# Optimization experiments

Hardware: AMD Instinct MI355X
Metric: run time of the kernel (lower is better)

## Reference

```python
import jax, jax.numpy as jnp
import numpy as np

B, S, D, H = 4, 2048, 1024, 16
HD = D // H
TEMP = 0.5
EPS = 1e-5


def setup_inputs() -> dict:
    key = jax.random.key(0)
    ks = jax.random.split(key, 9)
    s = 1.0 / np.sqrt(D)
    # weights stored as [in, out] (equivalent to torch Linear W.T)
    return {
        "x": jax.random.normal(ks[0], (B, S, D), dtype=jnp.float32),
        "Wq": jax.random.uniform(ks[1], (D, D), minval=-s, maxval=s),
        "bq": jnp.zeros((D,), jnp.float32),
        "Wk": jax.random.uniform(ks[2], (D, D), minval=-s, maxval=s),
        "bk": jnp.zeros((D,), jnp.float32),
        "Wv": jax.random.uniform(ks[3], (D, D), minval=-s, maxval=s),
        "bv": jnp.zeros((D,), jnp.float32),
        "Wo": jax.random.uniform(ks[4], (D, D), minval=-s, maxval=s),
        "bo": jnp.zeros((D,), jnp.float32),
        "ln_g": jnp.ones((D,), jnp.float32),
        "ln_b": jnp.zeros((D,), jnp.float32),
    }


def reference(x, Wq, bq, Wk, bk, Wv, bv, Wo, bo, ln_g, ln_b):
    # projections -> [B, H, S, HD]
    def proj(W, b):
        return (x @ W + b).reshape(B, S, H, HD).transpose(0, 2, 1, 3)

    Q, K, V = proj(Wq, bq), proj(Wk, bk), proj(Wv, bv)
    scale = 1.0 / (np.sqrt(HD) * TEMP)
    scores = jnp.einsum("bhqd,bhkd->bhqk", Q, K) * scale  # [B,H,S,S]
    attn = jax.nn.softmax(scores, axis=-1)  # dropout p=0 -> identity
    ctx = jnp.einsum("bhqk,bhkd->bhqd", attn, V)
    ctx = ctx.transpose(0, 2, 1, 3).reshape(B, S, D)
    out = ctx @ Wo + bo
    # layernorm(out + residual)
    h = out + x
    mu = h.mean(axis=-1, keepdims=True)
    var = h.var(axis=-1, keepdims=True)
    out = (h - mu) / jnp.sqrt(var + EPS) * ln_g + ln_b
    avg_attention = attn.mean(axis=1)  # [B, S, S]
    return out, avg_attention
```

## Files before the change

### kernel.cpp

```cpp
#include <hip/hip_runtime.h>

#define DEV static __device__ __forceinline__

typedef float f32x4 __attribute__((ext_vector_type(4)));
typedef __bf16 bf16x8 __attribute__((ext_vector_type(8)));
typedef unsigned short u16x8 __attribute__((ext_vector_type(8)));
typedef unsigned short u16x4 __attribute__((ext_vector_type(4)));
typedef unsigned u32x2 __attribute__((ext_vector_type(2)));

static constexpr float SCALE_LOG2E = 0.25f * 1.4426950408889634f;

DEV unsigned short f2bf(float f) {
  return __builtin_bit_cast(unsigned short, (__bf16)f);
}

DEV unsigned pk2(float a, float b) {
  unsigned short lo = f2bf(a), hi = f2bf(b);
  return (unsigned)lo | ((unsigned)hi << 16);
}

DEV f32x4 fzero() { f32x4 z; z[0] = z[1] = z[2] = z[3] = 0.f; return z; }

DEV void gll16(const void* g, void* l) {
  __builtin_amdgcn_global_load_lds((__attribute__((address_space(1))) void*)g,
                                   (__attribute__((address_space(3))) void*)l, 16, 0, 0);
}

DEV f32x4 mfma16(bf16x8 a, bf16x8 b, f32x4 c) {
  return __builtin_amdgcn_mfma_f32_16x16x32_bf16(a, b, c, 0, 0, 0);
}

__global__ __launch_bounds__(256) void k_cvt_x(const float* __restrict__ x,
                                               unsigned short* __restrict__ xb, int n) {
  int i = (blockIdx.x * 256 + threadIdx.x) * 4;
  if (i < n) {
    f32x4 v = *(const f32x4*)(x + i);
    u16x4 o;
    o[0] = f2bf(v[0]); o[1] = f2bf(v[1]); o[2] = f2bf(v[2]); o[3] = f2bf(v[3]);
    *(u16x4*)(xb + i) = o;
  }
}

__global__ __launch_bounds__(256) void k_cvt_wT(const float* __restrict__ w0,
                                                const float* __restrict__ w1,
                                                const float* __restrict__ w2,
                                                const float* __restrict__ w3,
                                                unsigned short* __restrict__ wt) {
  __shared__ float t[32][33];
  const float* w = blockIdx.z == 0 ? w0 : blockIdx.z == 1 ? w1 : blockIdx.z == 2 ? w2 : w3;
  unsigned short* dst = wt + (size_t)blockIdx.z * 1024 * 1024;
  int n0 = blockIdx.x * 32, k0 = blockIdx.y * 32;
  int tx = threadIdx.x, ty = threadIdx.y;
#pragma unroll
  for (int i = 0; i < 4; ++i)
    t[ty + 8 * i][tx] = w[(size_t)(k0 + ty + 8 * i) * 1024 + n0 + tx];
  __syncthreads();
#pragma unroll
  for (int i = 0; i < 4; ++i)
    dst[(size_t)(n0 + ty + 8 * i) * 1024 + k0 + tx] = f2bf(t[tx][ty + 8 * i]);
}

template <int MODE>
__global__ __launch_bounds__(256) void k_gemm(
    const unsigned short* __restrict__ A, const unsigned short* __restrict__ Bt,
    unsigned short* __restrict__ oq, unsigned short* __restrict__ ok,
    unsigned short* __restrict__ ov, const float* __restrict__ biasq,
    const float* __restrict__ biask, const float* __restrict__ biasv,
    float* __restrict__ outh, const float* __restrict__ xres,
    const float* __restrict__ biaso) {
  __shared__ unsigned short As[128 * 64];
  __shared__ unsigned short Bs[128 * 64];
  const int tid = threadIdx.x;
  const int w = tid >> 6, ln = tid & 63;
  const int kg = ln >> 4, l15 = ln & 15;
  const int wm = w >> 1, wn = w & 1;
  const long arow0 = (long)blockIdx.y * 128;
  const long brow0 = (long)blockIdx.x * 128;

  f32x4 acc[4][4];
#pragma unroll
  for (int m = 0; m < 4; ++m) {
#pragma unroll
    for (int n = 0; n < 4; ++n) acc[m][n] = fzero();
  }

  for (int kt = 0; kt < 16; ++kt) {
    __syncthreads();
#pragma unroll
    for (int rnd = 0; rnd < 4; ++rnd) {
      int slot = rnd * 256 + tid;
      int r = slot >> 3, ch = slot & 7;
      int gch = ch ^ (r & 7);
      gll16(A + (arow0 + r) * 1024 + kt * 64 + gch * 8, (char*)As + slot * 16);
      gll16(Bt + (brow0 + r) * 1024 + kt * 64 + gch * 8, (char*)Bs + slot * 16);
    }
    __syncthreads();
#pragma unroll
    for (int kk = 0; kk < 2; ++kk) {
      bf16x8 af[4], bfr[4];
#pragma unroll
      for (int m = 0; m < 4; ++m) {
        int row = wm * 64 + m * 16 + l15;
        int bir = (kk * 64 + kg * 16) ^ ((row & 7) << 4);
        af[m] = *(const bf16x8*)((const char*)As + row * 128 + bir);
      }
#pragma unroll
      for (int n = 0; n < 4; ++n) {
        int row = wn * 64 + n * 16 + l15;
        int bir = (kk * 64 + kg * 16) ^ ((row & 7) << 4);
        bfr[n] = *(const bf16x8*)((const char*)Bs + row * 128 + bir);
      }
#pragma unroll
      for (int m = 0; m < 4; ++m) {
#pragma unroll
        for (int n = 0; n < 4; ++n) acc[m][n] = mfma16(af[m], bfr[n], acc[m][n]);
      }
    }
  }

#pragma unroll
  for (int n = 0; n < 4; ++n) {
    int col = (int)brow0 + wn * 64 + n * 16 + l15;
    if (MODE == 0) {
      int which = col >> 10, nn = col & 1023;
      int hh = nn >> 6, dd = nn & 63;
      unsigned short* dst = which == 0 ? oq : which == 1 ? ok : ov;
      const float* bp = which == 0 ? biasq : which == 1 ? biask : biasv;
      float bias = bp[nn];
#pragma unroll
      for (int m = 0; m < 4; ++m) {
        int row0 = (int)arow0 + wm * 64 + m * 16 + kg * 4;
#pragma unroll
        for (int r = 0; r < 4; ++r) {
          int row = row0 + r;
          int bb = row >> 11, ss = row & 2047;
          dst[(((long)(bb * 16 + hh)) * 2048 + ss) * 64 + dd] =
              f2bf(acc[m][n][r] + bias);
        }
      }
    } else {
      float bias = biaso[col];
#pragma unroll
      for (int m = 0; m < 4; ++m) {
        long row0 = arow0 + wm * 64 + m * 16 + kg * 4;
#pragma unroll
        for (int r = 0; r < 4; ++r) {
          long row = row0 + r;
          outh[row * 1024 + col] = acc[m][n][r] + bias + xres[row * 1024 + col];
        }
      }
    }
  }
}

__global__ __launch_bounds__(256, 4) void k_flash(
    const unsigned short* __restrict__ Q, const unsigned short* __restrict__ K,
    const unsigned short* __restrict__ V, unsigned short* __restrict__ ctx,
    float* __restrict__ mrow, float* __restrict__ lrow) {
  __shared__ unsigned short Ks[64 * 64];
  __shared__ unsigned short Vt[64 * 64];
  __shared__ unsigned short Ps[4][16 * 64];
  const int tid = threadIdx.x, w = tid >> 6, ln = tid & 63;
  const int kg = ln >> 4, l15 = ln & 15;
  const int qt = blockIdx.x, hh = blockIdx.y, bb = blockIdx.z;
  const long bh = (long)bb * 16 + hh;
  const unsigned short* Qg = Q + bh * 2048 * 64;
  const unsigned short* Kg = K + bh * 2048 * 64;
  const unsigned short* Vg = V + bh * 2048 * 64;

  const int qrow = qt * 64 + w * 16 + l15;
  bf16x8 qf[2];
  qf[0] = *(const bf16x8*)(Qg + (long)qrow * 64 + kg * 8);
  qf[1] = *(const bf16x8*)(Qg + (long)qrow * 64 + 32 + kg * 8);

  f32x4 oacc[4];
#pragma unroll
  for (int nf = 0; nf < 4; ++nf) oacc[nf] = fzero();
  float m_run = -1e30f, l_run = 0.f;

  char* pw = (char*)Ps[w] + l15 * 128;
  const int swz = (l15 & 7) << 4;

  for (int kt = 0; kt < 32; ++kt) {
    __syncthreads();
#pragma unroll
    for (int rnd = 0; rnd < 2; ++rnd) {
      int slot = rnd * 256 + tid;
      int r = slot >> 3, ch = slot & 7;
      int gch = ch ^ (r & 7);
      gll16(Kg + ((long)kt * 64 + r) * 64 + gch * 8, (char*)Ks + slot * 16);
    }
    {
      int kp = tid & 31, ch = tid >> 5;
      int r0 = kp * 2;
      u16x8 v0 = *(const u16x8*)(Vg + ((long)kt * 64 + r0) * 64 + ch * 8);
      u16x8 v1 = *(const u16x8*)(Vg + ((long)kt * 64 + r0 + 1) * 64 + ch * 8);
#pragma unroll
      for (int i = 0; i < 8; ++i) {
        int c = ch * 8 + i;
        unsigned val = (unsigned)v0[i] | ((unsigned)v1[i] << 16);
        *(unsigned*)((char*)Vt + c * 128 + ((r0 * 2) ^ ((c & 7) << 4))) = val;
      }
    }
    __syncthreads();

    f32x4 st[4];
#pragma unroll
    for (int nf = 0; nf < 4; ++nf) st[nf] = fzero();
#pragma unroll
    for (int kk = 0; kk < 2; ++kk) {
#pragma unroll
      for (int nf = 0; nf < 4; ++nf) {
        int row = nf * 16 + l15;
        int bir = (kk * 64 + kg * 16) ^ ((row & 7) << 4);
        bf16x8 kb = *(const bf16x8*)((const char*)Ks + row * 128 + bir);
        st[nf] = mfma16(kb, qf[kk], st[nf]);
      }
    }

    float mx0 = fmaxf(fmaxf(st[0][0], st[0][1]), fmaxf(st[0][2], st[0][3]));
    float mx1 = fmaxf(fmaxf(st[1][0], st[1][1]), fmaxf(st[1][2], st[1][3]));
    float mx2 = fmaxf(fmaxf(st[2][0], st[2][1]), fmaxf(st[2][2], st[2][3]));
    float mx3 = fmaxf(fmaxf(st[3][0], st[3][1]), fmaxf(st[3][2], st[3][3]));
    float mx = fmaxf(fmaxf(mx0, mx1), fmaxf(mx2, mx3));
    mx = fmaxf(mx, __shfl_xor(mx, 16));
    mx = fmaxf(mx, __shfl_xor(mx, 32));
    mx *= SCALE_LOG2E;
    float mnew = fmaxf(m_run, mx);
    float alpha = exp2f(m_run - mnew);
    m_run = mnew;

    float sum = 0.f;
#pragma unroll
    for (int nf = 0; nf < 4; ++nf) {
      float p0 = exp2f(st[nf][0] * SCALE_LOG2E - m_run);
      float p1 = exp2f(st[nf][1] * SCALE_LOG2E - m_run);
      float p2 = exp2f(st[nf][2] * SCALE_LOG2E - m_run);
      float p3 = exp2f(st[nf][3] * SCALE_LOG2E - m_run);
      st[nf][0] = p0; st[nf][1] = p1; st[nf][2] = p2; st[nf][3] = p3;
      sum += (p0 + p1) + (p2 + p3);
    }
    sum += __shfl_xor(sum, 16);
    sum += __shfl_xor(sum, 32);
    l_run = l_run * alpha + sum;

#pragma unroll
    for (int nf = 0; nf < 4; ++nf) {
      u32x2 pv2;
      pv2[0] = pk2(st[nf][0], st[nf][1]);
      pv2[1] = pk2(st[nf][2], st[nf][3]);
      *(u32x2*)(pw + ((nf * 32 + kg * 8) ^ swz)) = pv2;
    }

#pragma unroll
    for (int nf = 0; nf < 4; ++nf) oacc[nf] *= alpha;

#pragma unroll
    for (int kk = 0; kk < 2; ++kk) {
      bf16x8 pb = *(const bf16x8*)(pw + ((kk * 64 + kg * 16) ^ swz));
#pragma unroll
      for (int nf = 0; nf < 4; ++nf) {
        int dd = nf * 16 + l15;
        int bir2 = (kk * 64 + kg * 16) ^ ((dd & 7) << 4);
        bf16x8 vb = *(const bf16x8*)((const char*)Vt + dd * 128 + bir2);
        oacc[nf] = mfma16(vb, pb, oacc[nf]);
      }
    }
  }

  float linv = 1.0f / l_run;
#pragma unroll
  for (int nf = 0; nf < 4; ++nf) {
    u16x4 o;
#pragma unroll
    for (int r = 0; r < 4; ++r) o[r] = f2bf(oacc[nf][r] * linv);
    *(u16x4*)(ctx + ((long)bb * 2048 + qrow) * 1024 + hh * 64 + nf * 16 + kg * 4) = o;
  }
  if (kg == 0) {
    mrow[bh * 2048 + qrow] = m_run;
    lrow[bh * 2048 + qrow] = l_run;
  }
}

__global__ __launch_bounds__(256) void k_avg(
    const unsigned short* __restrict__ Q, const unsigned short* __restrict__ K,
    const float* __restrict__ mrow, const float* __restrict__ lrow,
    float* __restrict__ avg) {
  __shared__ unsigned short Qs[64 * 64];
  __shared__ unsigned short Ks[64 * 64];
  const int tid = threadIdx.x, w = tid >> 6, ln = tid & 63;
  const int kg = ln >> 4, l15 = ln & 15;
  const int kt = blockIdx.x, qt = blockIdx.y, bb = blockIdx.z;

  f32x4 aacc[4];
#pragma unroll
  for (int nf = 0; nf < 4; ++nf) aacc[nf] = fzero();

  for (int hh = 0; hh < 16; ++hh) {
    const long bh = (long)bb * 16 + hh;
    const unsigned short* Qg = Q + bh * 2048 * 64;
    const unsigned short* Kg = K + bh * 2048 * 64;
    __syncthreads();
#pragma unroll
    for (int rnd = 0; rnd < 2; ++rnd) {
      int slot = rnd * 256 + tid;
      int r = slot >> 3, ch = slot & 7;
      int gch = ch ^ (r & 7);
      gll16(Qg + ((long)qt * 64 + r) * 64 + gch * 8, (char*)Qs + slot * 16);
      gll16(Kg + ((long)kt * 64 + r) * 64 + gch * 8, (char*)Ks + slot * 16);
    }
    __syncthreads();

    f32x4 sc[4];
#pragma unroll
    for (int nf = 0; nf < 4; ++nf) sc[nf] = fzero();
#pragma unroll
    for (int kk = 0; kk < 2; ++kk) {
      int arow = w * 16 + l15;
      int bir = (kk * 64 + kg * 16) ^ ((arow & 7) << 4);
      bf16x8 aq = *(const bf16x8*)((const char*)Qs + arow * 128 + bir);
#pragma unroll
      for (int nf = 0; nf < 4; ++nf) {
        int krow = nf * 16 + l15;
        int bir2 = (kk * 64 + kg * 16) ^ ((krow & 7) << 4);
        bf16x8 kb = *(const bf16x8*)((const char*)Ks + krow * 128 + bir2);
        sc[nf] = mfma16(aq, kb, sc[nf]);
      }
    }
#pragma unroll
    for (int r = 0; r < 4; ++r) {
      int qrow = qt * 64 + w * 16 + kg * 4 + r;
      float m = mrow[bh * 2048 + qrow];
      float linv = 1.0f / lrow[bh * 2048 + qrow];
#pragma unroll
      for (int nf = 0; nf < 4; ++nf)
        aacc[nf][r] += exp2f(sc[nf][r] * SCALE_LOG2E - m) * linv;
    }
  }
#pragma unroll
  for (int nf = 0; nf < 4; ++nf) {
#pragma unroll
    for (int r = 0; r < 4; ++r) {
      int qrow = qt * 64 + w * 16 + kg * 4 + r;
      int kcol = kt * 64 + nf * 16 + l15;
      avg[((long)bb * 2048 + qrow) * 2048 + kcol] = aacc[nf][r] * 0.0625f;
    }
  }
}

__global__ __launch_bounds__(256) void k_ln(float* __restrict__ io,
                                            const float* __restrict__ g,
                                            const float* __restrict__ bvec) {
  __shared__ float red[8];
  long row = blockIdx.x;
  float* p = io + row * 1024;
  int tid = threadIdx.x;
  f32x4 v = *(const f32x4*)(p + tid * 4);
  float s = v[0] + v[1] + v[2] + v[3];
  float ss = v[0] * v[0] + v[1] * v[1] + v[2] * v[2] + v[3] * v[3];
#pragma unroll
  for (int m = 1; m < 64; m <<= 1) {
    s += __shfl_xor(s, m);
    ss += __shfl_xor(ss, m);
  }
  int w = tid >> 6;
  if ((tid & 63) == 0) { red[w * 2] = s; red[w * 2 + 1] = ss; }
  __syncthreads();
  s = red[0] + red[2] + red[4] + red[6];
  ss = red[1] + red[3] + red[5] + red[7];
  float mu = s * (1.0f / 1024.0f);
  float var = ss * (1.0f / 1024.0f) - mu * mu;
  float rs = rsqrtf(var + 1e-5f);
  f32x4 o;
#pragma unroll
  for (int i = 0; i < 4; ++i) {
    int c = tid * 4 + i;
    o[i] = (v[i] - mu) * rs * g[c] + bvec[c];
  }
  *(f32x4*)(p + tid * 4) = o;
}

extern "C" void kernel_launch(void* const* d_in, const int* in_sizes, int n_in,
                              void* d_out, int out_size, void* d_ws, size_t ws_size,
                              hipStream_t stream) {
  (void)in_sizes; (void)n_in; (void)out_size; (void)ws_size;
  const float* x  = (const float*)d_in[0];
  const float* Wq = (const float*)d_in[1];
  const float* bq = (const float*)d_in[2];
  const float* Wk = (const float*)d_in[3];
  const float* bk = (const float*)d_in[4];
  const float* Wv = (const float*)d_in[5];
  const float* bv = (const float*)d_in[6];
  const float* Wo = (const float*)d_in[7];
  const float* bo = (const float*)d_in[8];
  const float* lg = (const float*)d_in[9];
  const float* lb = (const float*)d_in[10];
  float* out = (float*)d_out;
  float* avg = out + (long)8192 * 1024;

  char* ws = (char*)d_ws;
  unsigned short* xb  = (unsigned short*)(ws);
  unsigned short* wt  = (unsigned short*)(ws + ((size_t)16 << 20));
  unsigned short* Qb  = (unsigned short*)(ws + ((size_t)24 << 20));
  unsigned short* Kb  = (unsigned short*)(ws + ((size_t)40 << 20));
  unsigned short* Vb  = (unsigned short*)(ws + ((size_t)56 << 20));
  unsigned short* ctx = (unsigned short*)(ws + ((size_t)72 << 20));
  float* mrow = (float*)(ws + ((size_t)88 << 20));
  float* lrow = (float*)(ws + ((size_t)88 << 20) + ((size_t)1 << 19));

  k_cvt_x<<<dim3(8192), dim3(256), 0, stream>>>(x, xb, 8192 * 1024);
  k_cvt_wT<<<dim3(32, 32, 4), dim3(32, 8), 0, stream>>>(Wq, Wk, Wv, Wo, wt);
  k_gemm<0><<<dim3(24, 64), dim3(256), 0, stream>>>(
      xb, wt, Qb, Kb, Vb, bq, bk, bv, nullptr, nullptr, nullptr);
  k_flash<<<dim3(32, 16, 4), dim3(256), 0, stream>>>(Qb, Kb, Vb, ctx, mrow, lrow);
  k_avg<<<dim3(32, 32, 4), dim3(256), 0, stream>>>(Qb, Kb, mrow, lrow, avg);
  k_gemm<1><<<dim3(8, 64), dim3(256), 0, stream>>>(
      ctx, wt + (size_t)3 * 1024 * 1024, nullptr, nullptr, nullptr, nullptr, nullptr,
      nullptr, out, x, bo);
  k_ln<<<dim3(8192), dim3(256), 0, stream>>>(out, lg, lb);
}
```

Baseline: 516.4 us.

## Pre-transpose V, remap blocks across XCDs, and streamline flash/avg kernels

A separate kernel transposes V into a global [d, s] layout, so the flash kernel can fill LDS with async global_load_lds instead of a register transpose each tile. All grids become 1D, with block indices remapped so neighbouring tiles land on the same XCD for L2 reuse. The avg kernel loads Q fragments straight to registers instead of through LDS, precomputes 1/16 into the reciprocal, writes vectorised f32x4 stores and declares higher occupancy. exp2f is replaced by the hardware exp2 builtin, at the cost of an extra kernel launch and extra V traffic.

```diff
diff --git a/kernel.cpp b/kernel.cpp
--- a/kernel.cpp
+++ b/kernel.cpp
@@ -13,19 +13,17 @@
 DEV unsigned short f2bf(float f) {
   return __builtin_bit_cast(unsigned short, (__bf16)f);
 }
-
 DEV unsigned pk2(float a, float b) {
   unsigned short lo = f2bf(a), hi = f2bf(b);
   return (unsigned)lo | ((unsigned)hi << 16);
 }
-
+DEV float ex2(float x) { return __builtin_amdgcn_exp2f(x); }
 DEV f32x4 fzero() { f32x4 z; z[0] = z[1] = z[2] = z[3] = 0.f; return z; }
 
 DEV void gll16(const void* g, void* l) {
   __builtin_amdgcn_global_load_lds((__attribute__((address_space(1))) void*)g,
                                    (__attribute__((address_space(3))) void*)l, 16, 0, 0);
 }
-
 DEV f32x4 mfma16(bf16x8 a, bf16x8 b, f32x4 c) {
   return __builtin_amdgcn_mfma_f32_16x16x32_bf16(a, b, c, 0, 0, 0);
 }
@@ -60,6 +58,21 @@
     dst[(size_t)(n0 + ty + 8 * i) * 1024 + k0 + tx] = f2bf(t[tx][ty + 8 * i]);
 }
 
+__global__ __launch_bounds__(256) void k_vT(const unsigned short* __restrict__ V,
+                                            unsigned short* __restrict__ Vt) {
+  const long base = (long)blockIdx.y * 131072;
+  const int s0 = blockIdx.x * 64;
+  const int s = threadIdx.x & 63, dg = threadIdx.x >> 6;
+  const unsigned short* src = V + base + (long)(s0 + s) * 64 + dg * 16;
+  u16x8 a = *(const u16x8*)(src);
+  u16x8 b = *(const u16x8*)(src + 8);
+  unsigned short* dst = Vt + base + (long)(dg * 16) * 2048 + s0 + s;
+#pragma unroll
+  for (int i = 0; i < 8; ++i) dst[(long)i * 2048] = a[i];
+#pragma unroll
+  for (int i = 0; i < 8; ++i) dst[(long)(8 + i) * 2048] = b[i];
+}
+
 template <int MODE>
 __global__ __launch_bounds__(256) void k_gemm(
     const unsigned short* __restrict__ A, const unsigned short* __restrict__ Bt,
@@ -67,22 +80,23 @@
     unsigned short* __restrict__ ov, const float* __restrict__ biasq,
     const float* __restrict__ biask, const float* __restrict__ biasv,
     float* __restrict__ outh, const float* __restrict__ xres,
-    const float* __restrict__ biaso) {
+    const float* __restrict__ biaso, int nx) {
   __shared__ unsigned short As[128 * 64];
   __shared__ unsigned short Bs[128 * 64];
   const int tid = threadIdx.x;
   const int w = tid >> 6, ln = tid & 63;
   const int kg = ln >> 4, l15 = ln & 15;
   const int wm = w >> 1, wn = w & 1;
-  const long arow0 = (long)blockIdx.y * 128;
-  const long brow0 = (long)blockIdx.x * 128;
+  const int chunk = gridDim.x >> 3;
+  const int lin = (blockIdx.x & 7) * chunk + (blockIdx.x >> 3);
+  const long arow0 = (long)(lin / nx) * 128;
+  const long brow0 = (long)(lin % nx) * 128;
 
   f32x4 acc[4][4];
 #pragma unroll
-  for (int m = 0; m < 4; ++m) {
+  for (int m = 0; m < 4; ++m)
 #pragma unroll
     for (int n = 0; n < 4; ++n) acc[m][n] = fzero();
-  }
 
   for (int kt = 0; kt < 16; ++kt) {
     __syncthreads();
@@ -111,10 +125,9 @@
         bfr[n] = *(const bf16x8*)((const char*)Bs + row * 128 + bir);
       }
 #pragma unroll
-      for (int m = 0; m < 4; ++m) {
+      for (int m = 0; m < 4; ++m)
 #pragma unroll
         for (int n = 0; n < 4; ++n) acc[m][n] = mfma16(af[m], bfr[n], acc[m][n]);
-      }
     }
   }
 
@@ -155,68 +168,68 @@
 
 __global__ __launch_bounds__(256, 4) void k_flash(
     const unsigned short* __restrict__ Q, const unsigned short* __restrict__ K,
-    const unsigned short* __restrict__ V, unsigned short* __restrict__ ctx,
+    const unsigned short* __restrict__ Vtg, unsigned short* __restrict__ ctx,
     float* __restrict__ mrow, float* __restrict__ lrow) {
   __shared__ unsigned short Ks[64 * 64];
   __shared__ unsigned short Vt[64 * 64];
   __shared__ unsigned short Ps[4][16 * 64];
   const int tid = threadIdx.x, w = tid >> 6, ln = tid & 63;
   const int kg = ln >> 4, l15 = ln & 15;
-  const int qt = blockIdx.x, hh = blockIdx.y, bb = blockIdx.z;
+  const int lin = (blockIdx.x & 7) * 256 + (blockIdx.x >> 3);
+  const int qt = lin & 31, hh = (lin >> 5) & 15, bb = lin >> 9;
   const long bh = (long)bb * 16 + hh;
-  const unsigned short* Qg = Q + bh * 2048 * 64;
-  const unsigned short* Kg = K + bh * 2048 * 64;
-  const unsigned short* Vg = V + bh * 2048 * 64;
-
+  const unsigned short* Qg = Q + bh * 131072;
   const int qrow = qt * 64 + w * 16 + l15;
-  bf16x8 qf[2];
-  qf[0] = *(const bf16x8*)(Qg + (long)qrow * 64 + kg * 8);
-  qf[1] = *(const bf16x8*)(Qg + (long)qrow * 64 + 32 + kg * 8);
+  const bf16x8 qf0 = *(const bf16x8*)(Qg + (long)qrow * 64 + kg * 8);
+  const bf16x8 qf1 = *(const bf16x8*)(Qg + (long)qrow * 64 + 32 + kg * 8);
+
+  const int r0 = tid >> 3, gch = (tid & 7) ^ (r0 & 7);
+  const unsigned short* kp0 = K + bh * 131072 + r0 * 64 + gch * 8;
+  const unsigned short* kp1 = kp0 + 32 * 64;
+  const unsigned short* vp0 = Vtg + bh * 131072 + r0 * 2048 + gch * 8;
+  const unsigned short* vp1 = vp0 + 32 * 2048;
+  char* kl0 = (char*)Ks + tid * 16;
+  char* kl1 = kl0 + 4096;
+  char* vl0 = (char*)Vt + tid * 16;
+  char* vl1 = vl0 + 4096;
+
+  const int swz = (l15 & 7) << 4;
+  int bir[2];
+  bir[0] = (kg * 16) ^ swz;
+  bir[1] = (64 + kg * 16) ^ swz;
+  const char* ksb[4];
+  const char* vtb[4];
+#pragma unroll
+  for (int nf = 0; nf < 4; ++nf) {
+    ksb[nf] = (const char*)Ks + (nf * 16 + l15) * 128;
+    vtb[nf] = (const char*)Vt + (nf * 16 + l15) * 128;
+  }
+  char* pw = (char*)Ps[w] + l15 * 128;
 
   f32x4 oacc[4];
 #pragma unroll
   for (int nf = 0; nf < 4; ++nf) oacc[nf] = fzero();
   float m_run = -1e30f, l_run = 0.f;
 
-  char* pw = (char*)Ps[w] + l15 * 128;
-  const int swz = (l15 & 7) << 4;
-
   for (int kt = 0; kt < 32; ++kt) {
     __syncthreads();
-#pragma unroll
-    for (int rnd = 0; rnd < 2; ++rnd) {
-      int slot = rnd * 256 + tid;
-      int r = slot >> 3, ch = slot & 7;
-      int gch = ch ^ (r & 7);
-      gll16(Kg + ((long)kt * 64 + r) * 64 + gch * 8, (char*)Ks + slot * 16);
-    }
-    {
-      int kp = tid & 31, ch = tid >> 5;
-      int r0 = kp * 2;
-      u16x8 v0 = *(const u16x8*)(Vg + ((long)kt * 64 + r0) * 64 + ch * 8);
-      u16x8 v1 = *(const u16x8*)(Vg + ((long)kt * 64 + r0 + 1) * 64 + ch * 8);
-#pragma unroll
-      for (int i = 0; i < 8; ++i) {
-        int c = ch * 8 + i;
-        unsigned val = (unsigned)v0[i] | ((unsigned)v1[i] << 16);
-        *(unsigned*)((char*)Vt + c * 128 + ((r0 * 2) ^ ((c & 7) << 4))) = val;
-      }
-    }
+    gll16(kp0, kl0);
+    gll16(kp1, kl1);
+    gll16(vp0, vl0);
+    gll16(vp1, vl1);
+    kp0 += 4096; kp1 += 4096; vp0 += 64; vp1 += 64;
     __syncthreads();
 
     f32x4 st[4];
 #pragma unroll
     for (int nf = 0; nf < 4; ++nf) st[nf] = fzero();
 #pragma unroll
-    for (int kk = 0; kk < 2; ++kk) {
+    for (int kk = 0; kk < 2; ++kk)
 #pragma unroll
       for (int nf = 0; nf < 4; ++nf) {
-        int row = nf * 16 + l15;
-        int bir = (kk * 64 + kg * 16) ^ ((row & 7) << 4);
-        bf16x8 kb = *(const bf16x8*)((const char*)Ks + row * 128 + bir);
-        st[nf] = mfma16(kb, qf[kk], st[nf]);
-      }
-    }
+        bf16x8 kb = *(const bf16x8*)(ksb[nf] + bir[kk]);
+        st[nf] = mfma16(kb, kk ? qf1 : qf0, st[nf]);
+      }
 
     float mx0 = fmaxf(fmaxf(st[0][0], st[0][1]), fmaxf(st[0][2], st[0][3]));
     float mx1 = fmaxf(fmaxf(st[1][0], st[1][1]), fmaxf(st[1][2], st[1][3]));
@@ -227,16 +240,16 @@
     mx = fmaxf(mx, __shfl_xor(mx, 32));
     mx *= SCALE_LOG2E;
     float mnew = fmaxf(m_run, mx);
-    float alpha = exp2f(m_run - mnew);
+    float alpha = ex2(m_run - mnew);
     m_run = mnew;
 
     float sum = 0.f;
 #pragma unroll
     for (int nf = 0; nf < 4; ++nf) {
-      float p0 = exp2f(st[nf][0] * SCALE_LOG2E - m_run);
-      float p1 = exp2f(st[nf][1] * SCALE_LOG2E - m_run);
-      float p2 = exp2f(st[nf][2] * SCALE_LOG2E - m_run);
-      float p3 = exp2f(st[nf][3] * SCALE_LOG2E - m_run);
+      float p0 = ex2(st[nf][0] * SCALE_LOG2E - m_run);
+      float p1 = ex2(st[nf][1] * SCALE_LOG2E - m_run);
+      float p2 = ex2(st[nf][2] * SCALE_LOG2E - m_run);
+      float p3 = ex2(st[nf][3] * SCALE_LOG2E - m_run);
       st[nf][0] = p0; st[nf][1] = p1; st[nf][2] = p2; st[nf][3] = p3;
       sum += (p0 + p1) + (p2 + p3);
     }
@@ -257,12 +270,10 @@
 
 #pragma unroll
     for (int kk = 0; kk < 2; ++kk) {
-      bf16x8 pb = *(const bf16x8*)(pw + ((kk * 64 + kg * 16) ^ swz));
+      bf16x8 pb = *(const bf16x8*)(pw + bir[kk]);
 #pragma unroll
       for (int nf = 0; nf < 4; ++nf) {
-        int dd = nf * 16 + l15;
-        int bir2 = (kk * 64 + kg * 16) ^ ((dd & 7) << 4);
-        bf16x8 vb = *(const bf16x8*)((const char*)Vt + dd * 128 + bir2);
+        bf16x8 vb = *(const bf16x8*)(vtb[nf] + bir[kk]);
         oacc[nf] = mfma16(vb, pb, oacc[nf]);
       }
     }
@@ -282,70 +293,69 @@
   }
 }
 
-__global__ __launch_bounds__(256) void k_avg(
+__global__ __launch_bounds__(256, 4) void k_avg(
     const unsigned short* __restrict__ Q, const unsigned short* __restrict__ K,
     const float* __restrict__ mrow, const float* __restrict__ lrow,
     float* __restrict__ avg) {
-  __shared__ unsigned short Qs[64 * 64];
   __shared__ unsigned short Ks[64 * 64];
   const int tid = threadIdx.x, w = tid >> 6, ln = tid & 63;
   const int kg = ln >> 4, l15 = ln & 15;
-  const int kt = blockIdx.x, qt = blockIdx.y, bb = blockIdx.z;
+  const int lin = (blockIdx.x & 7) * 512 + (blockIdx.x >> 3);
+  const int kt = lin & 31, qt = (lin >> 5) & 31, bb = lin >> 10;
+  const int qrow = qt * 64 + w * 16 + l15;
+
+  const int r0 = tid >> 3, gch = (tid & 7) ^ (r0 & 7);
+  const unsigned short* kp0 = K + (long)bb * 16 * 131072 + kt * 4096 + r0 * 64 + gch * 8;
+  const unsigned short* kp1 = kp0 + 2048;
+  char* kl0 = (char*)Ks + tid * 16;
+  char* kl1 = kl0 + 4096;
+  const unsigned short* qp = Q + (long)bb * 16 * 131072 + (long)qrow * 64 + kg * 8;
+  const float* mp = mrow + (long)bb * 16 * 2048 + qrow;
+  const float* lp = lrow + (long)bb * 16 * 2048 + qrow;
+
+  const int swz = (l15 & 7) << 4;
+  int bir[2];
+  bir[0] = (kg * 16) ^ swz;
+  bir[1] = (64 + kg * 16) ^ swz;
+  const char* ksb[4];
+#pragma unroll
+  for (int nf = 0; nf < 4; ++nf) ksb[nf] = (const char*)Ks + (nf * 16 + l15) * 128;
 
   f32x4 aacc[4];
 #pragma unroll
   for (int nf = 0; nf < 4; ++nf) aacc[nf] = fzero();
 
   for (int hh = 0; hh < 16; ++hh) {
-    const long bh = (long)bb * 16 + hh;
-    const unsigned short* Qg = Q + bh * 2048 * 64;
-    const unsigned short* Kg = K + bh * 2048 * 64;
-    __syncthreads();
-#pragma unroll
-    for (int rnd = 0; rnd < 2; ++rnd) {
-      int slot = rnd * 256 + tid;
-      int r = slot >> 3, ch = slot & 7;
-      int gch = ch ^ (r & 7);
-      gll16(Qg + ((long)qt * 64 + r) * 64 + gch * 8, (char*)Qs + slot * 16);
-      gll16(Kg + ((long)kt * 64 + r) * 64 + gch * 8, (char*)Ks + slot * 16);
-    }
-    __syncthreads();
-
-    f32x4 sc[4];
-#pragma unroll
-    for (int nf = 0; nf < 4; ++nf) sc[nf] = fzero();
-#pragma unroll
-    for (int kk = 0; kk < 2; ++kk) {
-      int arow = w * 16 + l15;
-      int bir = (kk * 64 + kg * 16) ^ ((arow & 7) << 4);
-      bf16x8 aq = *(const bf16x8*)((const char*)Qs + arow * 128 + bir);
+    __syncthreads();
+    gll16(kp0, kl0);
+    gll16(kp1, kl1);
+    bf16x8 q0 = *(const bf16x8*)(qp);
+    bf16x8 q1 = *(const bf16x8*)(qp + 32);
+    float m = *mp;
+    float li = 0.0625f / *lp;
+    kp0 += 131072; kp1 += 131072; qp += 131072; mp += 2048; lp += 2048;
+    __syncthreads();
+
+    f32x4 st[4];
+#pragma unroll
+    for (int nf = 0; nf < 4; ++nf) st[nf] = fzero();
+#pragma unroll
+    for (int kk = 0; kk < 2; ++kk)
 #pragma unroll
       for (int nf = 0; nf < 4; ++nf) {
-        int krow = nf * 16 + l15;
-        int bir2 = (kk * 64 + kg * 16) ^ ((krow & 7) << 4);
-        bf16x8 kb = *(const bf16x8*)((const char*)Ks + krow * 128 + bir2);
-        sc[nf] = mfma16(aq, kb, sc[nf]);
-      }
-    }
-#pragma unroll
-    for (int r = 0; r < 4; ++r) {
-      int qrow = qt * 64 + w * 16 + kg * 4 + r;
-      float m = mrow[bh * 2048 + qrow];
-      float linv = 1.0f / lrow[bh * 2048 + qrow];
-#pragma unroll
-      for (int nf = 0; nf < 4; ++nf)
-        aacc[nf][r] += exp2f(sc[nf][r] * SCALE_LOG2E - m) * linv;
-    }
-  }
-#pragma unroll
-  for (int nf = 0; nf < 4; ++nf) {
-#pragma unroll
-    for (int r = 0; r < 4; ++r) {
-      int qrow = qt * 64 + w * 16 + kg * 4 + r;
-      int kcol = kt * 64 + nf * 16 + l15;
-      avg[((long)bb * 2048 + qrow) * 2048 + kcol] = aacc[nf][r] * 0.0625f;
-    }
-  }
+        bf16x8 kb = *(const bf16x8*)(ksb[nf] + bir[kk]);
+        st[nf] = mfma16(kb, kk ? q1 : q0, st[nf]);
+      }
+#pragma unroll
+    for (int nf = 0; nf < 4; ++nf)
+#pragma unroll
+      for (int r = 0; r < 4; ++r)
+        aacc[nf][r] += ex2(st[nf][r] * SCALE_LOG2E - m) * li;
+  }
+#pragma unroll
+  for (int nf = 0; nf < 4; ++nf)
+    *(f32x4*)(avg + ((long)bb * 2048 + qrow) * 2048 + kt * 64 + nf * 16 + kg * 4) =
+        aacc[nf];
 }
 
 __global__ __launch_bounds__(256) void k_ln(float* __restrict__ io,
@@ -400,6 +410,7 @@
 
   char* ws = (char*)d_ws;
   unsigned short* xb  = (unsigned short*)(ws);
+  unsigned short* vtg = (unsigned short*)(ws);
   unsigned short* wt  = (unsigned short*)(ws + ((size_t)16 << 20));
   unsigned short* Qb  = (unsigned short*)(ws + ((size_t)24 << 20));
   unsigned short* Kb  = (unsigned short*)(ws + ((size_t)40 << 20));
@@ -410,12 +421,13 @@
 
   k_cvt_x<<<dim3(8192), dim3(256), 0, stream>>>(x, xb, 8192 * 1024);
   k_cvt_wT<<<dim3(32, 32, 4), dim3(32, 8), 0, stream>>>(Wq, Wk, Wv, Wo, wt);
-  k_gemm<0><<<dim3(24, 64), dim3(256), 0, stream>>>(
-      xb, wt, Qb, Kb, Vb, bq, bk, bv, nullptr, nullptr, nullptr);
-  k_flash<<<dim3(32, 16, 4), dim3(256), 0, stream>>>(Qb, Kb, Vb, ctx, mrow, lrow);
-  k_avg<<<dim3(32, 32, 4), dim3(256), 0, stream>>>(Qb, Kb, mrow, lrow, avg);
-  k_gemm<1><<<dim3(8, 64), dim3(256), 0, stream>>>(
+  k_gemm<0><<<dim3(1536), dim3(256), 0, stream>>>(
+      xb, wt, Qb, Kb, Vb, bq, bk, bv, nullptr, nullptr, nullptr, 24);
+  k_vT<<<dim3(32, 64), dim3(256), 0, stream>>>(Vb, vtg);
+  k_flash<<<dim3(2048), dim3(256), 0, stream>>>(Qb, Kb, vtg, ctx, mrow, lrow);
+  k_avg<<<dim3(4096), dim3(256), 0, stream>>>(Qb, Kb, mrow, lrow, avg);
+  k_gemm<1><<<dim3(512), dim3(256), 0, stream>>>(
       ctx, wt + (size_t)3 * 1024 * 1024, nullptr, nullptr, nullptr, nullptr, nullptr,
-      nullptr, out, x, bo);
+      nullptr, out, x, bo, 8);
   k_ln<<<dim3(8192), dim3(256), 0, stream>>>(out, lg, lb);
 }
```

New measurement: 465.8 us. 1.11x faster.
